# Performance work log

Hardware: AMD Instinct MI355X
Metric: run time of the kernel (lower is better)

Reference implementation:

```python
import jax, jax.numpy as jnp
import numpy as np

B, S, D = 4, 2048, 1024
H, DK, DV = 16, 64, 64
SCALE = 8.0  # scaling_factor = sqrt(dk)


def setup_inputs() -> dict:
    key = jax.random.key(0)
    ks = jax.random.split(key, 9)
    s = 1.0 / np.sqrt(D)
    return {
        "q": jax.random.normal(ks[0], (B, S, D), jnp.float32),
        "k": jax.random.normal(ks[1], (B, S, D), jnp.float32),
        "v": jax.random.normal(ks[2], (B, S, D), jnp.float32),
        "Wq": jax.random.uniform(ks[3], (D, H * DK), jnp.float32, -s, s),
        "bq": jax.random.uniform(ks[4], (H * DK,), jnp.float32, -s, s),
        "Wk": jax.random.uniform(ks[5], (D, H * DK), jnp.float32, -s, s),
        "bk": jax.random.uniform(ks[6], (H * DK,), jnp.float32, -s, s),
        "Wv": jax.random.uniform(ks[7], (D, H * DV), jnp.float32, -s, s),
        "bv": jax.random.uniform(ks[8], (H * DV,), jnp.float32, -s, s),
    }


def reference(q, k, v, Wq, bq, Wk, bk, Wv, bv):
    # Linear projections, then split heads: [B,S,H*d] -> [B,S,H,d]
    qh = (q @ Wq + bq).reshape(B, S, H, DK)
    kh = (k @ Wk + bk).reshape(B, S, H, DK)
    vh = (v @ Wv + bv).reshape(B, S, H, DV)
    # scores: [B,H,Sq,Sk]
    e = jnp.einsum("bqhd,bkhd->bhqk", qh, kh) / SCALE
    attn = jax.nn.softmax(e, axis=-1)
    out = jnp.einsum("bhqk,bkhd->bqhd", attn, vh)  # [B,Sq,H,DV]
    return out.reshape(B, S, H * DV)  # dropout p=0 -> identity
```

## Files before the change

### kernel.cpp

```cpp
#include <hip/hip_runtime.h>
#include <hip/hip_bf16.h>


typedef unsigned short u16;
typedef unsigned int   u32;
typedef short bf16x8 __attribute__((ext_vector_type(8)));
typedef short bf16x4 __attribute__((ext_vector_type(4)));
typedef float f32x4  __attribute__((ext_vector_type(4)));
typedef u32   u32x4  __attribute__((ext_vector_type(4)));

#define S_TOT 2048
#define HD    1024
#define QK_SCALE 0.18033688f

#if __has_builtin(__builtin_amdgcn_exp2f)
#define EXP2(x) __builtin_amdgcn_exp2f(x)
#else
#define EXP2(x) exp2f(x)
#endif

__device__ __forceinline__ u16 f2bf(float f) {
  union { float f; unsigned u; } v; v.f = f;
  unsigned r = v.u + 0x7FFFu + ((v.u >> 16) & 1u);
  return (u16)(r >> 16);
}

__device__ __forceinline__ u32 cvt_pk_bf16(float lo, float hi) {
  u32 r;
  asm("v_cvt_pk_bf16_f32 %0, %1, %2" : "=v"(r) : "v"(lo), "v"(hi));
  return r;
}

__device__ __forceinline__ bf16x4 ds_tr16(unsigned a) {
  bf16x4 d;
  asm volatile("ds_read_b64_tr_b16 %0, %1" : "=v"(d) : "v"(a) : "memory");
  return d;
}

__device__ __forceinline__ void gld16(const u16* g, u16* l) {
  __builtin_amdgcn_global_load_lds(
      (const __attribute__((address_space(1))) u32*)g,
      (__attribute__((address_space(3))) u32*)l, 16, 0, 0);
}

#define LGKM_FENCE() do { asm volatile("s_waitcnt lgkmcnt(0)" ::: "memory"); \
                          __builtin_amdgcn_sched_barrier(0); } while (0)

__global__ __launch_bounds__(256)
void conv_kernel(const float* __restrict__ x0, const float* __restrict__ x1, const float* __restrict__ x2,
                 const float* __restrict__ w0, const float* __restrict__ w1, const float* __restrict__ w2,
                 u16* __restrict__ Xb, u16* __restrict__ Wt)
{
  const int z = blockIdx.y;
  const int t = threadIdx.x;
  if (blockIdx.x < 1024) {
    const float* X = z == 0 ? x0 : (z == 1 ? x1 : x2);
    u16* Xz = Xb + (size_t)z * 8388608;
    int tid = blockIdx.x * 256 + t;
#pragma unroll
    for (int i = 0; i < 8; ++i) {
      int c = tid + i * 262144;
      int row = c >> 8, k4 = (c & 255) * 4;
      const float4 xv = *(const float4*)&X[(size_t)row * 1024 + k4];
      int p = (k4 & ~31) + 8 * ((k4 & 15) >> 2) + 4 * ((k4 >> 4) & 1);
      bf16x4 sv = { (short)f2bf(xv.x), (short)f2bf(xv.y), (short)f2bf(xv.z), (short)f2bf(xv.w) };
      *(bf16x4*)&Xz[(size_t)row * 1024 + p] = sv;
    }
  } else {
    const float* W = z == 0 ? w0 : (z == 1 ? w1 : w2);
    u16* Wz = Wt + (size_t)z * 1048576;
    int tid = (blockIdx.x - 1024) * 256 + t;
#pragma unroll
    for (int i = 0; i < 8; ++i) {
      int c = tid + i * 32768;
      int k = c >> 8, n4 = (c & 255) * 4;
      const float4 wv = *(const float4*)&W[(size_t)k * 1024 + n4];
      int off = ((n4 >> 7) * 32 + (k >> 5)) * 4096 + ((n4 >> 4) & 7) * 512
              + ((k >> 4) & 1) * 256 + (k & 15) * 16 + (n4 & 15);
      bf16x4 sv = { (short)f2bf(wv.x), (short)f2bf(wv.y), (short)f2bf(wv.z), (short)f2bf(wv.w) };
      *(bf16x4*)&Wz[off] = sv;
    }
  }
}

__global__ __launch_bounds__(256)
void gemm_kernel(const u16* __restrict__ Xb, const u16* __restrict__ Wt,
                 const float* __restrict__ b0, const float* __restrict__ b1, const float* __restrict__ b2,
                 u16* __restrict__ o0, u16* __restrict__ o1, u16* __restrict__ vT)
{
  int p  = blockIdx.x + 8 * blockIdx.y + 512 * blockIdx.z;
  int wk = (p & 7) * 192 + (p >> 3);
  int nb = wk & 7, mb = (wk >> 3) & 63, z = wk >> 9;

  const u16* Xz = Xb + (size_t)z * 8388608;
  const u16* Wz = Wt + (size_t)z * 1048576;
  const float* BS = z == 0 ? b0 : (z == 1 ? b1 : b2);
  const float  osc = (z == 0) ? QK_SCALE : 1.0f;

  const int t = threadIdx.x;
  const int lane = t & 63, wid = t >> 6;
  const int g = lane >> 4, ln = lane & 15;
  const int mbase = mb * 128, nbase = nb * 128;

  __shared__ __align__(16) u16 Al[2][128 * 32];
  __shared__ __align__(16) u16 Bl[2][16 * 256];

  f32x4 acc[4][4];
#pragma unroll
  for (int i = 0; i < 4; ++i)
#pragma unroll
    for (int j = 0; j < 4; ++j) { acc[i][j][0]=0.f; acc[i][j][1]=0.f; acc[i][j][2]=0.f; acc[i][j][3]=0.f; }

  const u16* sa = Xz + (size_t)(mbase + (t >> 2)) * 1024 + (t & 3) * 8;
  const u16* sb = Wz + (size_t)(nb * 32) * 4096 + t * 8;
  u16* alw[2] = { &Al[0][wid * 512], &Al[1][wid * 512] };
  u16* blw[2] = { &Bl[0][wid * 512], &Bl[1][wid * 512] };

  auto stage = [&](int kb, int buf) __attribute__((always_inline)) {
    gld16(sa + kb * 32,               alw[buf]);
    gld16(sa + kb * 32 + 64 * 1024,   alw[buf] + 2048);
    gld16(sb + kb * 4096,             blw[buf]);
    gld16(sb + kb * 4096 + 2048,      blw[buf] + 2048);
  };

  stage(0, 0);
  __syncthreads();

  if (z < 2) {
    const int wm = wid >> 1, wn = wid & 1;
    u16* O = z == 0 ? o0 : o1;
    const unsigned bsb[2] = {
      (unsigned)(size_t)&Bl[0][0] + (unsigned)((wn * 4) * 1024) + lane * 8,
      (unsigned)(size_t)&Bl[1][0] + (unsigned)((wn * 4) * 1024) + lane * 8 };

    auto compute = [&](int cur) __attribute__((always_inline)) {
      bf16x8 af[4];
#pragma unroll
      for (int mf = 0; mf < 4; ++mf)
        af[mf] = *(const bf16x8*)&Al[cur][(wm * 64 + mf * 16 + ln) * 32 + g * 8];
      bf16x8 bfv[4];
#pragma unroll
      for (int nf = 0; nf < 4; ++nf) {
        bf16x4 lo = ds_tr16(bsb[cur] + (unsigned)(nf * 1024));
        bf16x4 hi = ds_tr16(bsb[cur] + (unsigned)(nf * 1024 + 512));
        bf16x8 bb;
        bb[0]=lo[0]; bb[1]=lo[1]; bb[2]=lo[2]; bb[3]=lo[3];
        bb[4]=hi[0]; bb[5]=hi[1]; bb[6]=hi[2]; bb[7]=hi[3];
        bfv[nf] = bb;
      }
      LGKM_FENCE();
      __builtin_amdgcn_s_setprio(1);
#pragma unroll
      for (int mf = 0; mf < 4; ++mf)
#pragma unroll
        for (int nf = 0; nf < 4; ++nf)
          acc[mf][nf] = __builtin_amdgcn_mfma_f32_16x16x32_bf16(af[mf], bfv[nf], acc[mf][nf], 0, 0, 0);
      __builtin_amdgcn_s_setprio(0);
    };

    for (int kb = 0; kb < 32; kb += 2) {
      if (kb + 1 < 32) stage(kb + 1, 1);
      compute(0);
      __syncthreads();
      if (kb + 2 < 32) stage(kb + 2, 0);
      compute(1);
      __syncthreads();
    }

#pragma unroll
    for (int nf = 0; nf < 4; ++nf) {
      int n = nbase + wn * 64 + nf * 16 + ln;
      float bv = BS[n];
#pragma unroll
      for (int mf = 0; mf < 4; ++mf)
#pragma unroll
        for (int r = 0; r < 4; ++r) {
          int m = mbase + wm * 64 + mf * 16 + 4 * g + r;
          O[(size_t)m * 1024 + n] = f2bf((acc[mf][nf][r] + bv) * osc);
        }
    }
  } else {
    const int wseq = wid >> 1, wdv = wid & 1;
    const unsigned bsb2[2] = {
      (unsigned)(size_t)&Bl[0][0] + (unsigned)((wdv * 4) * 1024) + lane * 8,
      (unsigned)(size_t)&Bl[1][0] + (unsigned)((wdv * 4) * 1024) + lane * 8 };

    auto compute2 = [&](int cur) __attribute__((always_inline)) {
      bf16x8 afw[4];
#pragma unroll
      for (int mf = 0; mf < 4; ++mf) {
        bf16x4 lo = ds_tr16(bsb2[cur] + (unsigned)(mf * 1024));
        bf16x4 hi = ds_tr16(bsb2[cur] + (unsigned)(mf * 1024 + 512));
        bf16x8 bb;
        bb[0]=lo[0]; bb[1]=lo[1]; bb[2]=lo[2]; bb[3]=lo[3];
        bb[4]=hi[0]; bb[5]=hi[1]; bb[6]=hi[2]; bb[7]=hi[3];
        afw[mf] = bb;
      }
      bf16x8 bfx[4];
#pragma unroll
      for (int nf = 0; nf < 4; ++nf)
        bfx[nf] = *(const bf16x8*)&Al[cur][(wseq * 64 + nf * 16 + ln) * 32 + g * 8];
      LGKM_FENCE();
      __builtin_amdgcn_s_setprio(1);
#pragma unroll
      for (int mf = 0; mf < 4; ++mf)
#pragma unroll
        for (int nf = 0; nf < 4; ++nf)
          acc[mf][nf] = __builtin_amdgcn_mfma_f32_16x16x32_bf16(afw[mf], bfx[nf], acc[mf][nf], 0, 0, 0);
      __builtin_amdgcn_s_setprio(0);
    };

    for (int kb = 0; kb < 32; kb += 2) {
      if (kb + 1 < 32) stage(kb + 1, 1);
      compute2(0);
      __syncthreads();
      if (kb + 2 < 32) stage(kb + 2, 0);
      compute2(1);
      __syncthreads();
    }

#pragma unroll
    for (int mf = 0; mf < 4; ++mf)
#pragma unroll
      for (int r = 0; r < 4; ++r) {
        int dvg = nbase + wdv * 64 + mf * 16 + 4 * g + r;
        float bv = BS[dvg];
        int hh = dvg >> 6, dvl = dvg & 63;
#pragma unroll
        for (int nf = 0; nf < 4; ++nf) {
          int m = mbase + wseq * 64 + nf * 16 + ln;
          int bb = m >> 11, ss = m & 2047;
          vT[((size_t)(bb * 16 + hh) * 64 + dvl) * 2048 + ss] = f2bf(acc[mf][nf][r] + bv);
        }
      }
  }
}

__global__ __launch_bounds__(256)
void proj_kernel(const float* __restrict__ x0, const float* __restrict__ x1, const float* __restrict__ x2,
                 const float* __restrict__ w0, const float* __restrict__ w1, const float* __restrict__ w2,
                 const float* __restrict__ b0, const float* __restrict__ b1, const float* __restrict__ b2,
                 u16* __restrict__ o0, u16* __restrict__ o1, u16* __restrict__ vT)
{
  int p  = blockIdx.x + 8 * blockIdx.y + 512 * blockIdx.z;
  int wk = (p & 7) * 192 + (p >> 3);
  int nb = wk & 7, mb = (wk >> 3) & 63, z = wk >> 9;

  const float* X  = z == 0 ? x0 : (z == 1 ? x1 : x2);
  const float* W  = z == 0 ? w0 : (z == 1 ? w1 : w2);
  const float* BS = z == 0 ? b0 : (z == 1 ? b1 : b2);
  const float  osc = (z == 0) ? QK_SCALE : 1.0f;

  const int t = threadIdx.x;
  const int lane = t & 63, wid = t >> 6;
  const int g = lane >> 4, ln = lane & 15;
  const int wm = wid >> 1, wn = wid & 1;
  const int mbase = mb * 128, nbase = nb * 128;

  __shared__ __align__(16) u16 As[128 * 40];
  __shared__ __align__(16) u16 Bs[16 * 272];

  f32x4 acc[4][4];
#pragma unroll
  for (int i = 0; i < 4; ++i)
#pragma unroll
    for (int j = 0; j < 4; ++j) { acc[i][j][0]=0.f; acc[i][j][1]=0.f; acc[i][j][2]=0.f; acc[i][j][3]=0.f; }

  const int arow = t >> 3;
  const int ak0  = (t & 7) * 4;
  const int ap   = 8 * ((ak0 & 15) >> 2) + 4 * (ak0 >> 4);
  const int bkr  = t >> 5;
  const int bnc  = (t & 31) * 4;
  const int bnblk = bnc >> 4, bncl = bnc & 15;

  const unsigned bs_base = (unsigned)(size_t)&Bs[0];

  for (int kb = 0; kb < 32; ++kb) {
    const int kbase = kb * 32;
#pragma unroll
    for (int ps = 0; ps < 4; ++ps) {
      int row = arow + 32 * ps;
      const float4 xv = *(const float4*)&X[(size_t)(mbase + row) * 1024 + kbase + ak0];
      bf16x4 sv = { (short)f2bf(xv.x), (short)f2bf(xv.y), (short)f2bf(xv.z), (short)f2bf(xv.w) };
      *(bf16x4*)&As[row * 40 + ap] = sv;
    }
#pragma unroll
    for (int ps = 0; ps < 4; ++ps) {
      int kr = bkr + 8 * ps;
      const float4 wv = *(const float4*)&W[(size_t)(kbase + kr) * 1024 + nbase + bnc];
      bf16x4 sv = { (short)f2bf(wv.x), (short)f2bf(wv.y), (short)f2bf(wv.z), (short)f2bf(wv.w) };
      *(bf16x4*)&Bs[(bnblk * 2 + (kr >> 4)) * 272 + (kr & 15) * 16 + bncl] = sv;
    }
    __syncthreads();

    bf16x8 af[4];
#pragma unroll
    for (int mf = 0; mf < 4; ++mf)
      af[mf] = *(const bf16x8*)&As[(wm * 64 + mf * 16 + ln) * 40 + g * 8];

    bf16x8 bfv[4];
#pragma unroll
    for (int nf = 0; nf < 4; ++nf) {
      unsigned base = bs_base + (unsigned)(((wn * 4 + nf) * 2) * 544) + lane * 8;
      bf16x4 lo = ds_tr16(base);
      bf16x4 hi = ds_tr16(base + 544);
      bf16x8 bb;
      bb[0]=lo[0]; bb[1]=lo[1]; bb[2]=lo[2]; bb[3]=lo[3];
      bb[4]=hi[0]; bb[5]=hi[1]; bb[6]=hi[2]; bb[7]=hi[3];
      bfv[nf] = bb;
    }
    LGKM_FENCE();
#pragma unroll
    for (int mf = 0; mf < 4; ++mf)
#pragma unroll
      for (int nf = 0; nf < 4; ++nf)
        acc[mf][nf] = __builtin_amdgcn_mfma_f32_16x16x32_bf16(af[mf], bfv[nf], acc[mf][nf], 0, 0, 0);
    __syncthreads();
  }

#pragma unroll
  for (int nf = 0; nf < 4; ++nf) {
    int n = nbase + wn * 64 + nf * 16 + ln;
    float bv = BS[n];
#pragma unroll
    for (int mf = 0; mf < 4; ++mf)
#pragma unroll
      for (int r = 0; r < 4; ++r) {
        int m = mbase + wm * 64 + mf * 16 + 4 * g + r;
        float val = (acc[mf][nf][r] + bv) * osc;
        if (z < 2) {
          u16* O = z == 0 ? o0 : o1;
          O[(size_t)m * 1024 + n] = f2bf(val);
        } else {
          vT[((size_t)((m >> 11) * 16 + (n >> 6)) * 64 + (n & 63)) * 2048 + (m & 2047)] = f2bf(val);
        }
      }
  }
}

__global__ __launch_bounds__(512)
void attn_kernel(const u16* __restrict__ qh, const u16* __restrict__ kh, const u16* __restrict__ vT,
                 float* __restrict__ out)
{
  int p  = blockIdx.x + 8 * blockIdx.y + 128 * blockIdx.z;
  int wk = (p & 7) * 64 + (p >> 3);
  int qt = wk & 7, h = (wk >> 3) & 15, b = wk >> 7;

  const int t = threadIdx.x;
  const int lane = t & 63, wid = t >> 6;
  const int g = lane >> 4, ln = lane & 15;
  const size_t bS = (size_t)b * S_TOT;
  const int qwin = qt * 256 + wid * 32;

  __shared__ __align__(16) u16 Ks[64 * 72];
  __shared__ __align__(16) u16 Vt[64 * 72];

  bf16x8 qf[2][2];
#pragma unroll
  for (int nf = 0; nf < 2; ++nf) {
    const u16* qrow = &qh[(bS + qwin + nf * 16 + ln) * HD + h * 64];
#pragma unroll
    for (int kk = 0; kk < 2; ++kk) {
      bf16x4 lo = *(const bf16x4*)&qrow[kk * 32 + 4 * g];
      bf16x4 hi = *(const bf16x4*)&qrow[kk * 32 + 4 * g + 16];
      bf16x8 qq;
      qq[0]=lo[0]; qq[1]=lo[1]; qq[2]=lo[2]; qq[3]=lo[3];
      qq[4]=hi[0]; qq[5]=hi[1]; qq[6]=hi[2]; qq[7]=hi[3];
      qf[nf][kk] = qq;
    }
  }

  bf16x8 ones;
#pragma unroll
  for (int j = 0; j < 8; ++j) ones[j] = (short)0x3F80;

  f32x4 o[2][4];
#pragma unroll
  for (int i = 0; i < 2; ++i)
#pragma unroll
    for (int j = 0; j < 4; ++j) { o[i][j][0]=0.f; o[i][j][1]=0.f; o[i][j][2]=0.f; o[i][j][3]=0.f; }
  f32x4 o1[2];
  o1[0][0]=0.f; o1[0][1]=0.f; o1[0][2]=0.f; o1[0][3]=0.f;
  o1[1][0]=0.f; o1[1][1]=0.f; o1[1][2]=0.f; o1[1][3]=0.f;

  const int skv = t >> 4;
  const int sd0 = (t & 15) * 4;
  const int kpos = 32 * (sd0 >> 5) + 8 * ((sd0 & 15) >> 2) + 4 * ((sd0 >> 4) & 1);
  u16* ksw[2];
  ksw[0] = &Ks[skv * 72 + kpos];
  ksw[1] = &Ks[(skv + 32) * 72 + kpos];
  const u16* kp = &kh[(bS + skv) * HD + h * 64 + sd0];

  const int vdv  = t >> 3;
  const int vkv8 = (t & 7) * 8;
  const int vp0  = 32 * (vkv8 >> 5) + 8 * ((vkv8 & 15) >> 2) + 4 * ((vkv8 >> 4) & 1);
  const int vkv4 = vkv8 + 4;
  const int vp1  = 32 * (vkv4 >> 5) + 8 * ((vkv4 & 15) >> 2) + 4 * ((vkv4 >> 4) & 1);
  u16* vsw0 = &Vt[vdv * 72 + vp0];
  u16* vsw1 = &Vt[vdv * 72 + vp1];
  const u16* vp = &vT[((size_t)(b * 16 + h) * 64 + vdv) * 2048 + vkv8];

  const size_t KSTEP = (size_t)64 * HD, C32 = (size_t)32 * HD;

  bf16x4 kr[2];
  kr[0] = *(const bf16x4*)kp; kr[1] = *(const bf16x4*)(kp + C32);
  bf16x8 vr = *(const bf16x8*)vp;
  kp += KSTEP; vp += 64;

  for (int it = 0; it < 32; ++it) {
    *(bf16x4*)ksw[0] = kr[0];
    *(bf16x4*)ksw[1] = kr[1];
    bf16x4 vlo = { vr[0], vr[1], vr[2], vr[3] };
    bf16x4 vhi = { vr[4], vr[5], vr[6], vr[7] };
    *(bf16x4*)vsw0 = vlo;
    *(bf16x4*)vsw1 = vhi;
    __syncthreads();

    if (it < 31) {
      kr[0] = *(const bf16x4*)kp; kr[1] = *(const bf16x4*)(kp + C32);
      vr = *(const bf16x8*)vp;
      kp += KSTEP; vp += 64;
    }

#pragma unroll
    for (int s = 0; s < 2; ++s) {
      bf16x8 kf[2][2];
#pragma unroll
      for (int mf = 0; mf < 2; ++mf)
#pragma unroll
        for (int kk = 0; kk < 2; ++kk)
          kf[mf][kk] = *(const bf16x8*)&Ks[(s * 32 + mf * 16 + ln) * 72 + kk * 32 + 8 * g];

      f32x4 sc[2][2];
      __builtin_amdgcn_s_setprio(1);
#pragma unroll
      for (int mf = 0; mf < 2; ++mf)
#pragma unroll
        for (int nf = 0; nf < 2; ++nf) {
          f32x4 a; a[0]=0.f; a[1]=0.f; a[2]=0.f; a[3]=0.f;
#pragma unroll
          for (int kk = 0; kk < 2; ++kk)
            a = __builtin_amdgcn_mfma_f32_16x16x32_bf16(kf[mf][kk], qf[nf][kk], a, 0, 0, 0);
          sc[mf][nf] = a;
        }
      __builtin_amdgcn_s_setprio(0);

      bf16x8 vf[4];
#pragma unroll
      for (int nf = 0; nf < 4; ++nf)
        vf[nf] = *(const bf16x8*)&Vt[(nf * 16 + ln) * 72 + s * 32 + 8 * g];

      bf16x8 pa[2];
#pragma unroll
      for (int nf = 0; nf < 2; ++nf) {
        float pv[2][4];
#pragma unroll
        for (int mf = 0; mf < 2; ++mf)
#pragma unroll
          for (int r = 0; r < 4; ++r)
            pv[mf][r] = EXP2(sc[mf][nf][r]);
        union { u32x4 u; bf16x8 b; } pk;
        pk.u[0] = cvt_pk_bf16(pv[0][0], pv[0][1]);
        pk.u[1] = cvt_pk_bf16(pv[0][2], pv[0][3]);
        pk.u[2] = cvt_pk_bf16(pv[1][0], pv[1][1]);
        pk.u[3] = cvt_pk_bf16(pv[1][2], pv[1][3]);
        pa[nf] = pk.b;
      }

      __builtin_amdgcn_s_setprio(1);
#pragma unroll
      for (int mq = 0; mq < 2; ++mq) {
#pragma unroll
        for (int nf = 0; nf < 4; ++nf)
          o[mq][nf] = __builtin_amdgcn_mfma_f32_16x16x32_bf16(pa[mq], vf[nf], o[mq][nf], 0, 0, 0);
        o1[mq] = __builtin_amdgcn_mfma_f32_16x16x32_bf16(pa[mq], ones, o1[mq], 0, 0, 0);
      }
      __builtin_amdgcn_s_setprio(0);
    }
    __syncthreads();
  }

#pragma unroll
  for (int mq = 0; mq < 2; ++mq)
#pragma unroll
    for (int r = 0; r < 4; ++r) {
      float inv = 1.0f / o1[mq][r];
      int qrow = qwin + mq * 16 + 4 * g + r;
#pragma unroll
      for (int nf = 0; nf < 4; ++nf)
        out[(bS + qrow) * HD + h * 64 + nf * 16 + ln] = o[mq][nf][r] * inv;
    }
}

extern "C" void kernel_launch(void* const* d_in, const int* in_sizes, int n_in,
                              void* d_out, int out_size, void* d_ws, size_t ws_size,
                              hipStream_t stream) {
  const float* q  = (const float*)d_in[0];
  const float* k  = (const float*)d_in[1];
  const float* v  = (const float*)d_in[2];
  const float* Wq = (const float*)d_in[3];
  const float* bq = (const float*)d_in[4];
  const float* Wk = (const float*)d_in[5];
  const float* bk = (const float*)d_in[6];
  const float* Wv = (const float*)d_in[7];
  const float* bv = (const float*)d_in[8];
  float* out = (float*)d_out;

  u16* qh = (u16*)d_ws;
  u16* kh = qh + (size_t)8192 * 1024;
  u16* vT = kh + (size_t)8192 * 1024;

  const size_t XB_OFF = (size_t)3 * 8192 * 1024;
  const size_t WT_OFF = XB_OFF + (size_t)3 * 8192 * 1024;
  const size_t NEED   = (WT_OFF + (size_t)3 * 1024 * 1024) * 2;

  if (ws_size >= NEED) {
    u16* Xb = (u16*)d_ws + XB_OFF;
    u16* Wt = (u16*)d_ws + WT_OFF;
    conv_kernel<<<dim3(1152, 3), 256, 0, stream>>>(q, k, v, Wq, Wk, Wv, Xb, Wt);
    gemm_kernel<<<dim3(8, 64, 3), 256, 0, stream>>>(Xb, Wt, bq, bk, bv, qh, kh, vT);
  } else {
    proj_kernel<<<dim3(8, 64, 3), 256, 0, stream>>>(q, k, v, Wq, Wk, Wv, bq, bk, bv, qh, kh, vT);
  }
  attn_kernel<<<dim3(8, 16, 4), 512, 0, stream>>>(qh, kh, vT, out);
}
```

Before: 171.8 us.

## Pre-transpose and XOR-swizzle weight layout, replace ds_read_tr with plain LDS reads

```diff
diff --git a/kernel.cpp b/kernel.cpp
--- a/kernel.cpp
+++ b/kernel.cpp
@@ -63,6 +63,7 @@
       int row = c >> 8, k4 = (c & 255) * 4;
       const float4 xv = *(const float4*)&X[(size_t)row * 1024 + k4];
       int p = (k4 & ~31) + 8 * ((k4 & 15) >> 2) + 4 * ((k4 >> 4) & 1);
+      p ^= (row & 6) << 2;
       bf16x4 sv = { (short)f2bf(xv.x), (short)f2bf(xv.y), (short)f2bf(xv.z), (short)f2bf(xv.w) };
       *(bf16x4*)&Xz[(size_t)row * 1024 + p] = sv;
     }
@@ -73,11 +74,16 @@
 #pragma unroll
     for (int i = 0; i < 8; ++i) {
       int c = tid + i * 32768;
-      int k = c >> 8, n4 = (c & 255) * 4;
-      const float4 wv = *(const float4*)&W[(size_t)k * 1024 + n4];
-      int off = ((n4 >> 7) * 32 + (k >> 5)) * 4096 + ((n4 >> 4) & 7) * 512
-              + ((k >> 4) & 1) * 256 + (k & 15) * 16 + (n4 & 15);
-      bf16x4 sv = { (short)f2bf(wv.x), (short)f2bf(wv.y), (short)f2bf(wv.z), (short)f2bf(wv.w) };
+      int n = c & 1023, k4 = (c >> 10) * 4;
+      float wv0 = W[(size_t)(k4 + 0) * 1024 + n];
+      float wv1 = W[(size_t)(k4 + 1) * 1024 + n];
+      float wv2 = W[(size_t)(k4 + 2) * 1024 + n];
+      float wv3 = W[(size_t)(k4 + 3) * 1024 + n];
+      int kl = k4 & 31;
+      int kp = 8 * ((kl & 15) >> 2) + 4 * ((kl >> 4) & 1);
+      int off = ((n >> 7) * 32 + (k4 >> 5)) * 4096 + (n & 127) * 32
+              + (kp ^ ((n & 6) << 2));
+      bf16x4 sv = { (short)f2bf(wv0), (short)f2bf(wv1), (short)f2bf(wv2), (short)f2bf(wv3) };
       *(bf16x4*)&Wz[off] = sv;
     }
   }
@@ -101,9 +107,10 @@
   const int lane = t & 63, wid = t >> 6;
   const int g = lane >> 4, ln = lane & 15;
   const int mbase = mb * 128, nbase = nb * 128;
+  const int xr = (ln & 6) << 2;
 
   __shared__ __align__(16) u16 Al[2][128 * 32];
-  __shared__ __align__(16) u16 Bl[2][16 * 256];
+  __shared__ __align__(16) u16 Bl[2][128 * 32];
 
   f32x4 acc[4][4];
 #pragma unroll
@@ -129,26 +136,15 @@
   if (z < 2) {
     const int wm = wid >> 1, wn = wid & 1;
     u16* O = z == 0 ? o0 : o1;
-    const unsigned bsb[2] = {
-      (unsigned)(size_t)&Bl[0][0] + (unsigned)((wn * 4) * 1024) + lane * 8,
-      (unsigned)(size_t)&Bl[1][0] + (unsigned)((wn * 4) * 1024) + lane * 8 };
 
     auto compute = [&](int cur) __attribute__((always_inline)) {
-      bf16x8 af[4];
+      bf16x8 af[4], bfv[4];
 #pragma unroll
       for (int mf = 0; mf < 4; ++mf)
-        af[mf] = *(const bf16x8*)&Al[cur][(wm * 64 + mf * 16 + ln) * 32 + g * 8];
-      bf16x8 bfv[4];
-#pragma unroll
-      for (int nf = 0; nf < 4; ++nf) {
-        bf16x4 lo = ds_tr16(bsb[cur] + (unsigned)(nf * 1024));
-        bf16x4 hi = ds_tr16(bsb[cur] + (unsigned)(nf * 1024 + 512));
-        bf16x8 bb;
-        bb[0]=lo[0]; bb[1]=lo[1]; bb[2]=lo[2]; bb[3]=lo[3];
-        bb[4]=hi[0]; bb[5]=hi[1]; bb[6]=hi[2]; bb[7]=hi[3];
-        bfv[nf] = bb;
-      }
-      LGKM_FENCE();
+        af[mf] = *(const bf16x8*)&Al[cur][(wm * 64 + mf * 16 + ln) * 32 + (g * 8 ^ xr)];
+#pragma unroll
+      for (int nf = 0; nf < 4; ++nf)
+        bfv[nf] = *(const bf16x8*)&Bl[cur][(wn * 64 + nf * 16 + ln) * 32 + (g * 8 ^ xr)];
       __builtin_amdgcn_s_setprio(1);
 #pragma unroll
       for (int mf = 0; mf < 4; ++mf)
@@ -181,26 +177,15 @@
     }
   } else {
     const int wseq = wid >> 1, wdv = wid & 1;
-    const unsigned bsb2[2] = {
-      (unsigned)(size_t)&Bl[0][0] + (unsigned)((wdv * 4) * 1024) + lane * 8,
-      (unsigned)(size_t)&Bl[1][0] + (unsigned)((wdv * 4) * 1024) + lane * 8 };
 
     auto compute2 = [&](int cur) __attribute__((always_inline)) {
-      bf16x8 afw[4];
-#pragma unroll
-      for (int mf = 0; mf < 4; ++mf) {
-        bf16x4 lo = ds_tr16(bsb2[cur] + (unsigned)(mf * 1024));
-        bf16x4 hi = ds_tr16(bsb2[cur] + (unsigned)(mf * 1024 + 512));
-        bf16x8 bb;
-        bb[0]=lo[0]; bb[1]=lo[1]; bb[2]=lo[2]; bb[3]=lo[3];
-        bb[4]=hi[0]; bb[5]=hi[1]; bb[6]=hi[2]; bb[7]=hi[3];
-        afw[mf] = bb;
-      }
-      bf16x8 bfx[4];
+      bf16x8 afw[4], bfx[4];
+#pragma unroll
+      for (int mf = 0; mf < 4; ++mf)
+        afw[mf] = *(const bf16x8*)&Bl[cur][(wdv * 64 + mf * 16 + ln) * 32 + (g * 8 ^ xr)];
 #pragma unroll
       for (int nf = 0; nf < 4; ++nf)
-        bfx[nf] = *(const bf16x8*)&Al[cur][(wseq * 64 + nf * 16 + ln) * 32 + g * 8];
-      LGKM_FENCE();
+        bfx[nf] = *(const bf16x8*)&Al[cur][(wseq * 64 + nf * 16 + ln) * 32 + (g * 8 ^ xr)];
       __builtin_amdgcn_s_setprio(1);
 #pragma unroll
       for (int mf = 0; mf < 4; ++mf)
```

Result: no change. 171.2 us (-0.3%).
